# Kernel optimization log

Measured on AMD Instinct MI355X. Metric: run time of the kernel, lower is better.

Reference implementation:

```python
import math
import jax, jax.numpy as jnp
import numpy as np

N, D, TOP_K = 8192, 256, 32
CAUSAL_ALPHA = 1.0

def setup_inputs() -> dict:
    key = jax.random.key(0)
    ks = jax.random.split(key, 8)
    s = 0.02  # weight init scale
    return {
        "x": jax.random.normal(ks[0], (N, D), jnp.float32),
        "mask": jnp.ones((N, N), dtype=bool),
        "causal_matrix": jax.random.uniform(ks[1], (N, N), jnp.float32),
        "Wq": jax.random.normal(ks[2], (D, D), jnp.float32) * s,
        "bq": jnp.zeros((D,), jnp.float32),
        "Wk": jax.random.normal(ks[3], (D, D), jnp.float32) * s,
        "bk": jnp.zeros((D,), jnp.float32),
        "Wv": jax.random.normal(ks[4], (D, D), jnp.float32) * s,
        "bv": jnp.zeros((D,), jnp.float32),
        "Wg": jax.random.normal(ks[5], (D, 2 * D), jnp.float32) * s,
        "bg": jnp.zeros((D,), jnp.float32),
    }

def reference(x, mask, causal_matrix, Wq, bq, Wk, bk, Wv, bv, Wg, bg):
    d = x.shape[-1]
    q = x @ Wq.T + bq          # [N, D]
    k = x @ Wk.T + bk
    v = x @ Wv.T + bv
    scores = (q @ k.T) / math.sqrt(d)                       # [N, N]
    scores = scores + CAUSAL_ALPHA * jnp.log(jnp.clip(causal_matrix, 1e-6))
    neg_inf = jnp.asarray(-jnp.inf, scores.dtype)
    scores = jnp.where(mask, scores, neg_inf)
    # top-k masking: keep only top-k entries per row, rest -> -inf
    topk_vals, topk_idx = jax.lax.top_k(scores, TOP_K)      # [N, K]
    rows = jnp.arange(scores.shape[0])[:, None]
    scores = jnp.full_like(scores, neg_inf).at[rows, topk_idx].set(topk_vals)
    weights = jax.nn.softmax(scores, axis=-1)               # [N, N]
    fused = weights @ v                                     # [N, D]
    gate = jax.nn.sigmoid(jnp.concatenate([x, fused], axis=-1) @ Wg.T + bg)
    out = gate * x + (1.0 - gate) * fused
    return out, weights
```

## Files before the change

### kernel.cpp

```cpp
#include <hip/hip_runtime.h>

#define NN 8192
#define DD 256
#define TOPK 32
#define SSTRIP 32
#define SW 256

typedef __attribute__((ext_vector_type(8))) short short8v;
typedef __attribute__((ext_vector_type(4))) float floatx4;

__device__ __forceinline__ unsigned short f2bf(float f) {
  union { float f; unsigned int u; } x;
  x.f = f;
  unsigned int r = x.u + 0x7FFFu + ((x.u >> 16) & 1u);
  return (unsigned short)(r >> 16);
}
__device__ __forceinline__ unsigned short f2h(float f) {
  _Float16 h = (_Float16)f;
  return __builtin_bit_cast(unsigned short, h);
}
__device__ __forceinline__ float h2f(unsigned short u) {
  return (float)__builtin_bit_cast(_Float16, u);
}
__device__ __forceinline__ unsigned int hkey(unsigned int u) {
  return (u & 0x8000u) ? ((~u) & 0xFFFFu) : (u | 0x8000u);
}
__device__ __forceinline__ size_t tile_off(int row, int j) {
  return ((size_t)(row >> 4) * 4096) + (size_t)(((j >> 5) * 512) +
         ((row & 15) * 32) + (((j >> 3) & 3) * 8) + (j & 7));
}

__global__ __launch_bounds__(256) void conv_kernel(
    const float* __restrict__ x,
    const float* __restrict__ Wq, const float* __restrict__ Wk,
    const float* __restrict__ Wv, const float* __restrict__ Wg,
    unsigned short* __restrict__ xb, unsigned short* __restrict__ wqkvb,
    unsigned short* __restrict__ wgb) {
  int g = blockIdx.x * 256 + threadIdx.x;
  const float* src;
  unsigned short* dst;
  int e;
  if (g < 524288) {
    e = g * 4; src = x + e; dst = xb + e;
  } else if (g < 524288 + 49152) {
    int e2 = (g - 524288) * 4;
    int which = e2 >> 16;
    int off = e2 & 65535;
    src = ((which == 0) ? Wq : (which == 1) ? Wk : Wv) + off;
    dst = wqkvb + which * 65536 + off;
  } else {
    int e3 = (g - 524288 - 49152) * 4;
    src = Wg + e3; dst = wgb + e3;
  }
  float4 f4 = *(const float4*)src;
  dst[0] = f2bf(f4.x); dst[1] = f2bf(f4.y);
  dst[2] = f2bf(f4.z); dst[3] = f2bf(f4.w);
}

__global__ __launch_bounds__(256) void qkv_kernel(
    const unsigned short* __restrict__ xb,
    const unsigned short* __restrict__ wqkvb,
    const float* __restrict__ bq, const float* __restrict__ bk,
    const float* __restrict__ bvb,
    unsigned short* __restrict__ qb, unsigned short* __restrict__ kb,
    float* __restrict__ v) {
  int tid = threadIdx.x;
  int w = tid >> 6, lane = tid & 63;
  int quad = lane >> 4, l16 = lane & 15;
  int rb = blockIdx.y * 128;
  int cs = blockIdx.x * 128;
  int cb = cs + blockIdx.z * 32;

  short8v afrag[2][8];
#pragma unroll
  for (int rh = 0; rh < 2; rh++)
#pragma unroll
    for (int kbi = 0; kbi < 8; kbi++) {
      int row = rb + w * 32 + rh * 16 + l16;
      afrag[rh][kbi] =
          *(const short8v*)(xb + (size_t)row * 256 + kbi * 32 + quad * 8);
    }

  floatx4 zero4 = {0.0f, 0.0f, 0.0f, 0.0f};
  floatx4 acc[2][2];
  acc[0][0] = zero4; acc[0][1] = zero4; acc[1][0] = zero4; acc[1][1] = zero4;
#pragma unroll
  for (int kbi = 0; kbi < 8; kbi++) {
    short8v b0 = *(const short8v*)(wqkvb + (size_t)(cb + l16) * 256 + kbi * 32 + quad * 8);
    short8v b1 = *(const short8v*)(wqkvb + (size_t)(cb + 16 + l16) * 256 + kbi * 32 + quad * 8);
    acc[0][0] = __builtin_amdgcn_mfma_f32_16x16x32_bf16(afrag[0][kbi], b0, acc[0][0], 0, 0, 0);
    acc[0][1] = __builtin_amdgcn_mfma_f32_16x16x32_bf16(afrag[0][kbi], b1, acc[0][1], 0, 0, 0);
    acc[1][0] = __builtin_amdgcn_mfma_f32_16x16x32_bf16(afrag[1][kbi], b0, acc[1][0], 0, 0, 0);
    acc[1][1] = __builtin_amdgcn_mfma_f32_16x16x32_bf16(afrag[1][kbi], b1, acc[1][1], 0, 0, 0);
  }
#pragma unroll
  for (int rh = 0; rh < 2; rh++)
#pragma unroll
    for (int ch = 0; ch < 2; ch++)
#pragma unroll
      for (int r = 0; r < 4; r++) {
        int row = rb + w * 32 + rh * 16 + quad * 4 + r;
        int col = cb + ch * 16 + l16;
        int which = col >> 8;
        int j = col & 255;
        const float* bias = (which == 0) ? bq : (which == 1) ? bk : bvb;
        float val = acc[rh][ch][r] + bias[j];
        if (which == 0)      qb[tile_off(row, j)] = f2bf(val * 0.0625f);
        else if (which == 1) kb[tile_off(row, j)] = f2bf(val);
        else                 v[(size_t)row * 256 + j] = val;
      }
}

__global__ __launch_bounds__(256) void score_kernel(
    const unsigned short* __restrict__ qb,
    const unsigned short* __restrict__ kb,
    const float* __restrict__ causal,
    float* __restrict__ weights) {
  int tid = threadIdx.x;
  int w = tid >> 6, lane = tid & 63;
  int quad = lane >> 4, l16 = lane & 15;
  int rb = blockIdx.y * 128;
  int cs = blockIdx.x * SW;
  int fragoff = l16 * 32 + quad * 8;

  short8v afrag[2][8];
#pragma unroll
  for (int rh = 0; rh < 2; rh++) {
    int gA = (rb + w * 32 + rh * 16) >> 4;
#pragma unroll
    for (int kbi = 0; kbi < 8; kbi++)
      afrag[rh][kbi] =
          *(const short8v*)(qb + (size_t)gA * 4096 + kbi * 512 + fragoff);
  }

  floatx4 zero4 = {0.0f, 0.0f, 0.0f, 0.0f};
  for (int it = 0; it < SW / 32; it++) {
    int cb = cs + it * 32;

    float cpre[2][4][2];
#pragma unroll
    for (int rh = 0; rh < 2; rh++)
#pragma unroll
      for (int r = 0; r < 4; r++) {
        int grow = rb + w * 32 + rh * 16 + quad * 4 + r;
        cpre[rh][r][0] = causal[(size_t)grow * NN + cb + l16];
        cpre[rh][r][1] = causal[(size_t)grow * NN + cb + 16 + l16];
      }

    const unsigned short* kbase = kb + (size_t)(cb >> 4) * 4096 + fragoff;
    floatx4 acc[2][2];
    acc[0][0] = zero4; acc[0][1] = zero4; acc[1][0] = zero4; acc[1][1] = zero4;
#pragma unroll
    for (int kbi = 0; kbi < 8; kbi++) {
      short8v b0 = *(const short8v*)(kbase + kbi * 512);
      short8v b1 = *(const short8v*)(kbase + 4096 + kbi * 512);
      acc[0][0] = __builtin_amdgcn_mfma_f32_16x16x32_bf16(afrag[0][kbi], b0, acc[0][0], 0, 0, 0);
      acc[0][1] = __builtin_amdgcn_mfma_f32_16x16x32_bf16(afrag[0][kbi], b1, acc[0][1], 0, 0, 0);
      acc[1][0] = __builtin_amdgcn_mfma_f32_16x16x32_bf16(afrag[1][kbi], b0, acc[1][0], 0, 0, 0);
      acc[1][1] = __builtin_amdgcn_mfma_f32_16x16x32_bf16(afrag[1][kbi], b1, acc[1][1], 0, 0, 0);
    }
#pragma unroll
    for (int rh = 0; rh < 2; rh++)
#pragma unroll
      for (int r = 0; r < 4; r++) {
        int grow = rb + w * 32 + rh * 16 + quad * 4 + r;
        float s0 = acc[rh][0][r] + __logf(fmaxf(cpre[rh][r][0], 1e-6f));
        float s1 = acc[rh][1][r] + __logf(fmaxf(cpre[rh][r][1], 1e-6f));
        unsigned int pk = (unsigned int)f2h(s0) | ((unsigned int)f2h(s1) << 16);
        unsigned short* sbrow = (unsigned short*)(weights + (size_t)grow * NN);
        *(unsigned int*)(sbrow + cb + l16 * 2) = pk;
      }
  }
}

__global__ __launch_bounds__(256) void topk_kernel(
    const float* __restrict__ weights,
    int* __restrict__ selC, float* __restrict__ selWt) {
  __shared__ int part[72];
  __shared__ int part2[8];
  __shared__ int selCol[TOPK];
  __shared__ float selSc[TOPK];

  int tid = threadIdx.x;
  int w = tid >> 6, lane = tid & 63;
  int row = blockIdx.x;
  const unsigned short* sb = (const unsigned short*)(weights + (size_t)row * NN);

  uint4 raw[4];
#pragma unroll
  for (int c = 0; c < 4; c++)
    raw[c] = *(const uint4*)(sb + c * 2048 + tid * 8);
  unsigned int keys[16];
#pragma unroll
  for (int c = 0; c < 4; c++) {
    unsigned int rr[4] = {raw[c].x, raw[c].y, raw[c].z, raw[c].w};
#pragma unroll
    for (int u = 0; u < 4; u++) {
      unsigned int klo = hkey(rr[u] & 0xFFFFu);
      unsigned int khi = hkey(rr[u] >> 16);
      keys[c * 4 + u] = klo | (khi << 16);
    }
  }

  int lo = 0, hi = 65535;
#pragma unroll 1
  for (int it = 0; it < 16; it++) {
    unsigned int mid = (unsigned int)((lo + hi) >> 1);
    int cnt = 0;
#pragma unroll
    for (int u = 0; u < 16; u++) {
      cnt += ((keys[u] & 0xFFFFu) > mid);
      cnt += ((keys[u] >> 16) > mid);
    }
#pragma unroll
    for (int off = 32; off >= 1; off >>= 1) cnt += __shfl_xor(cnt, off, 64);
    if (lane == 0) part[it * 4 + w] = cnt;
    __syncthreads();
    int tot = part[it * 4] + part[it * 4 + 1] + part[it * 4 + 2] + part[it * 4 + 3];
    if (lo < hi) { if (tot < TOPK) hi = (int)mid; else lo = (int)mid + 1; }
  }
  unsigned int K = (unsigned int)lo;

  {
    int cnt = 0;
#pragma unroll
    for (int u = 0; u < 16; u++) {
      cnt += ((keys[u] & 0xFFFFu) > K);
      cnt += ((keys[u] >> 16) > K);
    }
#pragma unroll
    for (int off = 32; off >= 1; off >>= 1) cnt += __shfl_xor(cnt, off, 64);
    if (lane == 0) part[64 + w] = cnt;
  }
  __syncthreads();
  int nGt = part[64] + part[65] + part[66] + part[67];

  int cGt = 0, cEq = 0;
#pragma unroll
  for (int u = 0; u < 16; u++) {
    unsigned int a = keys[u] & 0xFFFFu, b = keys[u] >> 16;
    cGt += (a > K) + (b > K);
    cEq += (a == K) + (b == K);
  }
  int sGt = cGt;
#pragma unroll
  for (int off = 1; off < 64; off <<= 1) {
    int t = __shfl_up(sGt, off, 64);
    if (lane >= off) sGt += t;
  }
  if (lane == 63) part2[w] = sGt;
  int sEq = cEq;
#pragma unroll
  for (int off = 1; off < 64; off <<= 1) {
    int t = __shfl_up(sEq, off, 64);
    if (lane >= off) sEq += t;
  }
  if (lane == 63) part2[4 + w] = sEq;
  __syncthreads();
  int offGt = 0, offEq = 0;
  for (int j = 0; j < w; j++) { offGt += part2[j]; offEq += part2[4 + j]; }
  int posG = offGt + sGt - cGt;
  int posT = nGt + offEq + sEq - cEq;

#pragma unroll
  for (int c = 0; c < 4; c++) {
    unsigned int rr[4] = {raw[c].x, raw[c].y, raw[c].z, raw[c].w};
#pragma unroll
    for (int e = 0; e < 8; e++) {
      unsigned int u16 = (e & 1) ? (rr[e >> 1] >> 16) : (rr[e >> 1] & 0xFFFFu);
      unsigned int k = hkey(u16);
      if (k > K || (k == K && posT < TOPK)) {
        int p = c * 2048 + tid * 8 + e;
        int g = p >> 5, wi = p & 31;
        int col = (g << 5) + ((wi & 1) << 4) + (wi >> 1);
        int slot = (k > K) ? posG : posT;
        selCol[slot] = col;
        selSc[slot] = h2f((unsigned short)u16);
      }
      if (k > K) posG++;
      else if (k == K) posT++;
    }
  }
  __syncthreads();

  if (tid < TOPK) {
    float s = selSc[tid];
    float m = s;
#pragma unroll
    for (int off = 16; off >= 1; off >>= 1) m = fmaxf(m, __shfl_xor(m, off, 64));
    float e = __expf(s - m);
    float Z = e;
#pragma unroll
    for (int off = 16; off >= 1; off >>= 1) Z += __shfl_xor(Z, off, 64);
    selC[(size_t)row * TOPK + tid] = selCol[tid];
    selWt[(size_t)row * TOPK + tid] = e / Z;
  }
}

__global__ __launch_bounds__(256) void fill_gather_kernel(
    const int* __restrict__ selC, const float* __restrict__ selWt,
    float* __restrict__ weights, const float* __restrict__ v,
    float* __restrict__ fused, unsigned short* __restrict__ fb) {
  __shared__ int sc[TOPK];
  __shared__ float sw[TOPK];
  int tid = threadIdx.x;
  int row = blockIdx.x;
  if (tid < TOPK) {
    sc[tid] = selC[(size_t)row * TOPK + tid];
    sw[tid] = selWt[(size_t)row * TOPK + tid];
  }

  float* wrow = weights + (size_t)row * NN;
  float4 z4 = {0.0f, 0.0f, 0.0f, 0.0f};
#pragma unroll
  for (int c = 0; c < 8; c++) *(float4*)(wrow + c * 1024 + tid * 4) = z4;
  __syncthreads();
  if (tid < TOPK) wrow[sc[tid]] = sw[tid];

  float acc = 0.0f;
#pragma unroll
  for (int i = 0; i < TOPK; i++)
    acc += sw[i] * v[(size_t)sc[i] * DD + tid];
  fused[(size_t)row * DD + tid] = acc;
  fb[(size_t)row * DD + tid] = f2bf(acc);
}

__global__ __launch_bounds__(256) void gate_kernel(
    const unsigned short* __restrict__ xb, const unsigned short* __restrict__ fb,
    const unsigned short* __restrict__ wgb, const float* __restrict__ bg,
    const float* __restrict__ x, const float* __restrict__ fused,
    float* __restrict__ out) {
  int tid = threadIdx.x;
  int w = tid >> 6, lane = tid & 63;
  int quad = lane >> 4, l16 = lane & 15;
  int rb = blockIdx.y * 128;
  int cs = blockIdx.x * 16;

  floatx4 acc[2];
  acc[0] = (floatx4){0.f, 0.f, 0.f, 0.f};
  acc[1] = (floatx4){0.f, 0.f, 0.f, 0.f};

#pragma unroll 1
  for (int kc = 0; kc < 2; kc++) {
    const unsigned short* asrc = kc ? fb : xb;
    short8v afrag[2][8];
#pragma unroll
    for (int rh = 0; rh < 2; rh++)
#pragma unroll
      for (int kbi = 0; kbi < 8; kbi++) {
        int row = rb + w * 32 + rh * 16 + l16;
        afrag[rh][kbi] =
            *(const short8v*)(asrc + (size_t)row * 256 + kbi * 32 + quad * 8);
      }
#pragma unroll
    for (int kbi = 0; kbi < 8; kbi++) {
      int col = cs + l16;
      short8v b = *(const short8v*)(wgb + (size_t)col * 512 + kc * 256 + kbi * 32 + quad * 8);
      acc[0] = __builtin_amdgcn_mfma_f32_16x16x32_bf16(afrag[0][kbi], b, acc[0], 0, 0, 0);
      acc[1] = __builtin_amdgcn_mfma_f32_16x16x32_bf16(afrag[1][kbi], b, acc[1], 0, 0, 0);
    }
  }
#pragma unroll
  for (int rh = 0; rh < 2; rh++)
#pragma unroll
    for (int r = 0; r < 4; r++) {
      int row = rb + w * 32 + rh * 16 + quad * 4 + r;
      int col = cs + l16;
      float t = acc[rh][r] + bg[col];
      float g = 1.0f / (1.0f + __expf(-t));
      size_t o = (size_t)row * 256 + col;
      out[o] = g * x[o] + (1.0f - g) * fused[o];
    }
}

extern "C" void kernel_launch(void* const* d_in, const int* in_sizes, int n_in,
                              void* d_out, int out_size, void* d_ws, size_t ws_size,
                              hipStream_t stream) {
  const float* x      = (const float*)d_in[0];
  const float* causal = (const float*)d_in[2];
  const float* Wq = (const float*)d_in[3];
  const float* bq = (const float*)d_in[4];
  const float* Wk = (const float*)d_in[5];
  const float* bk = (const float*)d_in[6];
  const float* Wv = (const float*)d_in[7];
  const float* bv = (const float*)d_in[8];
  const float* Wg = (const float*)d_in[9];
  const float* bg = (const float*)d_in[10];

  float* out = (float*)d_out;
  float* weights = out + (size_t)NN * DD;

  char* ws = (char*)d_ws;
  unsigned short* xb    = (unsigned short*)(ws);
  unsigned short* wqkvb = (unsigned short*)(ws + (4u << 20));
  unsigned short* wgb   = (unsigned short*)(ws + (4u << 20) + (512u << 10));
  unsigned short* qb    = (unsigned short*)(ws + (5u << 20));
  unsigned short* kb    = (unsigned short*)(ws + (9u << 20));
  float* v     = (float*)(ws + (13u << 20));
  float* fused = (float*)(ws + (21u << 20));
  unsigned short* fb = (unsigned short*)(ws + (29u << 20));
  int*   selC  = (int*)(ws + (5u << 20));
  float* selWt = (float*)(ws + (9u << 20));

  conv_kernel<<<dim3(2368), 256, 0, stream>>>(x, Wq, Wk, Wv, Wg, xb, wqkvb, wgb);
  qkv_kernel<<<dim3(6, 64, 4), 256, 0, stream>>>(xb, wqkvb, bq, bk, bv, qb, kb, v);
  score_kernel<<<dim3(SSTRIP, 64), 256, 0, stream>>>(qb, kb, causal, weights);
  topk_kernel<<<dim3(NN), 256, 0, stream>>>(weights, selC, selWt);
  fill_gather_kernel<<<dim3(NN), 256, 0, stream>>>(selC, selWt, weights, v, fused, fb);
  gate_kernel<<<dim3(16, 64), 256, 0, stream>>>(xb, fb, wgb, bg, x, fused, out);
}
```

Measured before the change: 873.8 us.

## Precompute fp16 log(causal) in a separate pass and permute K rows

Adds a clog_kernel that reads the causal matrix with fully coalesced float4 loads, takes the clamped log, and stores it as fp16 in the unused upper half of each weights row. score_kernel then reads these 2-byte logs, prefetched one iteration ahead, instead of strided fp32 causal values with a log per element. K rows are also permuted at write time so packed score columns come out in natural order, which removes the column remapping in topk. The cost is a full extra pass over the N×N causal matrix plus a fp16 intermediate write and re-read, and the log term is rounded to fp16 before the add.

```diff
diff --git a/kernel.cpp b/kernel.cpp
--- a/kernel.cpp
+++ b/kernel.cpp
@@ -57,6 +57,21 @@
   dst[2] = f2bf(f4.z); dst[3] = f2bf(f4.w);
 }
 
+__global__ __launch_bounds__(256) void clog_kernel(
+    const float* __restrict__ causal, float* __restrict__ weights) {
+  size_t g = (size_t)blockIdx.x * 256 + threadIdx.x;
+  size_t e = g * 4;
+  int row = (int)(e >> 13);
+  int col = (int)(e & 8191);
+  float4 c = *(const float4*)(causal + e);
+  unsigned int lo = (unsigned int)f2h(__logf(fmaxf(c.x, 1e-6f))) |
+                    ((unsigned int)f2h(__logf(fmaxf(c.y, 1e-6f))) << 16);
+  unsigned int hi = (unsigned int)f2h(__logf(fmaxf(c.z, 1e-6f))) |
+                    ((unsigned int)f2h(__logf(fmaxf(c.w, 1e-6f))) << 16);
+  unsigned short* crow = (unsigned short*)(weights + (size_t)row * NN + 4096);
+  *(uint2*)(crow + col) = make_uint2(lo, hi);
+}
+
 __global__ __launch_bounds__(256) void qkv_kernel(
     const unsigned short* __restrict__ xb,
     const unsigned short* __restrict__ wqkvb,
@@ -105,16 +120,20 @@
         int j = col & 255;
         const float* bias = (which == 0) ? bq : (which == 1) ? bk : bvb;
         float val = acc[rh][ch][r] + bias[j];
-        if (which == 0)      qb[tile_off(row, j)] = f2bf(val * 0.0625f);
-        else if (which == 1) kb[tile_off(row, j)] = f2bf(val);
-        else                 v[(size_t)row * 256 + j] = val;
+        if (which == 0) {
+          qb[tile_off(row, j)] = f2bf(val * 0.0625f);
+        } else if (which == 1) {
+          int S = (row & ~31) | ((row & 1) << 4) | ((row & 31) >> 1);
+          kb[tile_off(S, j)] = f2bf(val);
+        } else {
+          v[(size_t)row * 256 + j] = val;
+        }
       }
 }
 
 __global__ __launch_bounds__(256) void score_kernel(
     const unsigned short* __restrict__ qb,
     const unsigned short* __restrict__ kb,
-    const float* __restrict__ causal,
     float* __restrict__ weights) {
   int tid = threadIdx.x;
   int w = tid >> 6, lane = tid & 63;
@@ -133,21 +152,27 @@
           *(const short8v*)(qb + (size_t)gA * 4096 + kbi * 512 + fragoff);
   }
 
+  const unsigned short* crow[2][4];
+#pragma unroll
+  for (int rh = 0; rh < 2; rh++)
+#pragma unroll
+    for (int r = 0; r < 4; r++) {
+      int grow = rb + w * 32 + rh * 16 + quad * 4 + r;
+      crow[rh][r] = (const unsigned short*)(weights + (size_t)grow * NN + 4096);
+    }
+
+  unsigned int ccur[2][4];
+#pragma unroll
+  for (int rh = 0; rh < 2; rh++)
+#pragma unroll
+    for (int r = 0; r < 4; r++)
+      ccur[rh][r] = *(const unsigned int*)(crow[rh][r] + cs + 2 * l16);
+
   floatx4 zero4 = {0.0f, 0.0f, 0.0f, 0.0f};
   for (int it = 0; it < SW / 32; it++) {
     int cb = cs + it * 32;
-
-    float cpre[2][4][2];
-#pragma unroll
-    for (int rh = 0; rh < 2; rh++)
-#pragma unroll
-      for (int r = 0; r < 4; r++) {
-        int grow = rb + w * 32 + rh * 16 + quad * 4 + r;
-        cpre[rh][r][0] = causal[(size_t)grow * NN + cb + l16];
-        cpre[rh][r][1] = causal[(size_t)grow * NN + cb + 16 + l16];
-      }
-
     const unsigned short* kbase = kb + (size_t)(cb >> 4) * 4096 + fragoff;
+
     floatx4 acc[2][2];
     acc[0][0] = zero4; acc[0][1] = zero4; acc[1][0] = zero4; acc[1][1] = zero4;
 #pragma unroll
@@ -159,17 +184,33 @@
       acc[1][0] = __builtin_amdgcn_mfma_f32_16x16x32_bf16(afrag[1][kbi], b0, acc[1][0], 0, 0, 0);
       acc[1][1] = __builtin_amdgcn_mfma_f32_16x16x32_bf16(afrag[1][kbi], b1, acc[1][1], 0, 0, 0);
     }
+
+    unsigned int cnxt[2][4];
+    if (it + 1 < SW / 32) {
+#pragma unroll
+      for (int rh = 0; rh < 2; rh++)
+#pragma unroll
+        for (int r = 0; r < 4; r++)
+          cnxt[rh][r] = *(const unsigned int*)(crow[rh][r] + cb + 32 + 2 * l16);
+    }
+
 #pragma unroll
     for (int rh = 0; rh < 2; rh++)
 #pragma unroll
       for (int r = 0; r < 4; r++) {
         int grow = rb + w * 32 + rh * 16 + quad * 4 + r;
-        float s0 = acc[rh][0][r] + __logf(fmaxf(cpre[rh][r][0], 1e-6f));
-        float s1 = acc[rh][1][r] + __logf(fmaxf(cpre[rh][r][1], 1e-6f));
+        float l0 = h2f((unsigned short)(ccur[rh][r] & 0xFFFFu));
+        float l1 = h2f((unsigned short)(ccur[rh][r] >> 16));
+        float s0 = acc[rh][0][r] + l0;
+        float s1 = acc[rh][1][r] + l1;
         unsigned int pk = (unsigned int)f2h(s0) | ((unsigned int)f2h(s1) << 16);
         unsigned short* sbrow = (unsigned short*)(weights + (size_t)grow * NN);
         *(unsigned int*)(sbrow + cb + l16 * 2) = pk;
       }
+#pragma unroll
+    for (int rh = 0; rh < 2; rh++)
+#pragma unroll
+      for (int r = 0; r < 4; r++) ccur[rh][r] = cnxt[rh][r];
   }
 }
 
@@ -271,10 +312,8 @@
       unsigned int k = hkey(u16);
       if (k > K || (k == K && posT < TOPK)) {
         int p = c * 2048 + tid * 8 + e;
-        int g = p >> 5, wi = p & 31;
-        int col = (g << 5) + ((wi & 1) << 4) + (wi >> 1);
         int slot = (k > K) ? posG : posT;
-        selCol[slot] = col;
+        selCol[slot] = p;
         selSc[slot] = h2f((unsigned short)u16);
       }
       if (k > K) posG++;
@@ -403,8 +442,9 @@
   float* selWt = (float*)(ws + (9u << 20));
 
   conv_kernel<<<dim3(2368), 256, 0, stream>>>(x, Wq, Wk, Wv, Wg, xb, wqkvb, wgb);
+  clog_kernel<<<dim3(65536), 256, 0, stream>>>(causal, weights);
   qkv_kernel<<<dim3(6, 64, 4), 256, 0, stream>>>(xb, wqkvb, bq, bk, bv, qb, kb, v);
-  score_kernel<<<dim3(SSTRIP, 64), 256, 0, stream>>>(qb, kb, causal, weights);
+  score_kernel<<<dim3(SSTRIP, 64), 256, 0, stream>>>(qb, kb, weights);
   topk_kernel<<<dim3(NN), 256, 0, stream>>>(weights, selC, selWt);
   fill_gather_kernel<<<dim3(NN), 256, 0, stream>>>(selC, selWt, weights, v, fused, fb);
   gate_kernel<<<dim3(16, 64), 256, 0, stream>>>(xb, fb, wgb, bg, x, fused, out);
```

Result: slower. 924.6 us (+5.8%).
